# Optimization experiments

Hardware: AMD Instinct MI355X
Metric: run time of the kernel (lower is better)

Reference implementation:

```python
import jax, jax.numpy as jnp
import numpy as np

ALPHA = 0.2      # LeakyReLU negative slope
DROPOUT_P = 0.1  # torch F.dropout default training=True, so it IS applied
D_OUT = 128


def setup_inputs() -> dict:
    key = jax.random.key(0)
    k1, k2, k3 = jax.random.split(key, 3)
    N, D_IN = 8192, 128
    batch = jax.random.normal(k1, (N, D_IN), dtype=jnp.float32)
    # xavier_uniform gain=1.414 scale for faithfulness of magnitude
    w = jax.random.uniform(k2, (D_IN, D_OUT), dtype=jnp.float32, minval=-1.0, maxval=1.0) * (1.414 * np.sqrt(6.0 / (D_IN + D_OUT)))
    a = jax.random.uniform(k3, (2 * D_OUT, 1), dtype=jnp.float32, minval=-1.0, maxval=1.0) * (1.414 * np.sqrt(6.0 / (2 * D_OUT + 1)))
    return {"batch": batch, "w": w, "a": a}


def reference(batch, w, a):
    h = batch.reshape(-1, w.shape[0])            # [N, D_in]
    Wh = h @ w                                   # [N, D_out]
    Wh1 = Wh @ a[:D_OUT, :]                      # [N, 1]
    Wh2 = Wh @ a[D_OUT:, :]                      # [N, 1]
    e = Wh1 + Wh2.T                              # [N, N] additive scores
    e = jnp.where(e > 0, e, ALPHA * e)           # LeakyReLU
    attention = jax.nn.softmax(e, axis=1)        # row softmax
    # dropout with a fixed key (deterministic reference)
    keep = jax.random.bernoulli(jax.random.key(42), 1.0 - DROPOUT_P, attention.shape)
    attention = jnp.where(keep, attention / (1.0 - DROPOUT_P), 0.0)
    h_prime = attention @ Wh                     # [N, D_out]
    return jax.nn.elu(h_prime)                   # concat=True -> elu
```

## Files before the change

kernel.cpp:

```cpp
#include <hip/hip_runtime.h>
#include <stdint.h>

#define ALPHA 0.2f
#define LOG2E 1.4426950408889634f

typedef __bf16 bf16x8 __attribute__((ext_vector_type(8)));
typedef float f32x4 __attribute__((ext_vector_type(4)));

__device__ __forceinline__ uint32_t rotl32(uint32_t x, int r) {
  return __builtin_amdgcn_alignbit(x, x, 32 - r);
}

__device__ __forceinline__ uint32_t tf_mix(uint32_t f) {
  const uint32_t ks1 = 42u, ks2 = 0x1BD11BF0u;
  uint32_t x0 = 0u;
  uint32_t x1 = f + ks1;
#define TFR(r) { x0 += x1; x1 = rotl32(x1, r); x1 ^= x0; }
  TFR(13) TFR(15) TFR(26) TFR(6)  x0 += ks1; x1 += ks2 + 1u;
  TFR(17) TFR(29) TFR(16) TFR(24) x0 += ks2; x1 += 0u  + 2u;
  TFR(13) TFR(15) TFR(26) TFR(6)  x0 += 0u;  x1 += ks1 + 3u;
  TFR(17) TFR(29) TFR(16) TFR(24) x0 += ks1; x1 += ks2 + 4u;
  TFR(13) TFR(15) TFR(26) TFR(6)  x0 += ks2; x1 += 0u  + 5u;
#undef TFR
  return x0 ^ x1;
}

__device__ __forceinline__ unsigned short f2bf(float f) {
  uint32_t u = __float_as_uint(f);
  return (unsigned short)((u + 0x7fffu + ((u >> 16) & 1u)) >> 16);
}

__global__ __launch_bounds__(256) void wh_kernel(
    const float* __restrict__ batch, const float* __restrict__ w,
    const float* __restrict__ a, unsigned short* __restrict__ whb2,
    float* __restrict__ s1, float* __restrict__ s2, uint32_t* __restrict__ s2key) {
  __shared__ float whlds[32][128];
  int t = threadIdx.x;
  int i0 = blockIdx.x * 32;
  int d = t & 127, rg = t >> 7;
  int ib = i0 + rg * 16;
  float acc[16];
#pragma unroll
  for (int r = 0; r < 16; ++r) acc[r] = 0.f;
  for (int k = 0; k < 128; k += 4) {
    float wv0 = w[(k + 0) * 128 + d];
    float wv1 = w[(k + 1) * 128 + d];
    float wv2 = w[(k + 2) * 128 + d];
    float wv3 = w[(k + 3) * 128 + d];
#pragma unroll
    for (int r = 0; r < 16; ++r) {
      float4 b4 = *(const float4*)&batch[(ib + r) * 128 + k];
      acc[r] = fmaf(b4.w, wv3, fmaf(b4.z, wv2, fmaf(b4.y, wv1, fmaf(b4.x, wv0, acc[r]))));
    }
  }
  unsigned short hb[16];
#pragma unroll
  for (int r = 0; r < 16; ++r) {
    whlds[rg * 16 + r][d] = acc[r];
    hb[r] = f2bf(acc[r]);
  }
  uint32_t pk[8];
#pragma unroll
  for (int q = 0; q < 8; ++q) pk[q] = (uint32_t)hb[2 * q] | ((uint32_t)hb[2 * q + 1] << 16);
  uint32_t base0 = (((uint32_t)(ib >> 3) * 16u + (uint32_t)(d & 15)) * 8u + (uint32_t)(d >> 4)) * 8u;
  *(uint4*)&whb2[base0]        = make_uint4(pk[0], pk[1], pk[2], pk[3]);
  *(uint4*)&whb2[base0 + 1024] = make_uint4(pk[4], pk[5], pk[6], pk[7]);
  __syncthreads();
  int rr = t >> 3, seg = t & 7, c0 = seg * 16;
  const float* wr = &whlds[rr][c0];
  float p1 = 0.f, p2 = 0.f;
#pragma unroll
  for (int c = 0; c < 16; ++c) {
    float v = wr[c];
    p1 = fmaf(v, a[c0 + c], p1);
    p2 = fmaf(v, a[128 + c0 + c], p2);
  }
  p1 += __shfl_xor(p1, 1, 64); p1 += __shfl_xor(p1, 2, 64); p1 += __shfl_xor(p1, 4, 64);
  p2 += __shfl_xor(p2, 1, 64); p2 += __shfl_xor(p2, 2, 64); p2 += __shfl_xor(p2, 4, 64);
  if (seg == 0) { s1[i0 + rr] = p1; s2[i0 + rr] = p2; }
  float v = (seg == 0) ? p2 : -3.4e38f;
#pragma unroll
  for (int m = 1; m <= 32; m <<= 1) v = fmaxf(v, __shfl_xor(v, m, 64));
  if ((t & 63) == 0) {
    uint32_t b = __float_as_uint(v);
    uint32_t key = (b & 0x80000000u) ? ~b : (b | 0x80000000u);
    atomicMax(s2key, key);
  }
}

__global__ __launch_bounds__(256, 4) void gat_main(
    const float* __restrict__ s1, const float* __restrict__ s2g,
    const uint32_t* __restrict__ s2key, const unsigned short* __restrict__ whb2,
    float* __restrict__ pacc, float* __restrict__ pz) {
  __shared__ __align__(16) float smem[4160];
  int t = threadIdx.x;
  int rb = blockIdx.x >> 2, ck = blockIdx.x & 3;
  int R0 = rb * 16, C0 = ck * 2048;

  for (int k = t; k < 512; k += 256) {
    float4 v4 = ((const float4*)(s2g + C0))[k];
    float sL, e1, e2;
    sL = v4.x * LOG2E; e1 = __builtin_amdgcn_exp2f(sL); e2 = __builtin_amdgcn_exp2f(ALPHA * sL);
    ((float2*)smem)[k * 4 + 0] = make_float2(e1, e2);
    sL = v4.y * LOG2E; e1 = __builtin_amdgcn_exp2f(sL); e2 = __builtin_amdgcn_exp2f(ALPHA * sL);
    ((float2*)smem)[k * 4 + 1] = make_float2(e1, e2);
    sL = v4.z * LOG2E; e1 = __builtin_amdgcn_exp2f(sL); e2 = __builtin_amdgcn_exp2f(ALPHA * sL);
    ((float2*)smem)[k * 4 + 2] = make_float2(e1, e2);
    sL = v4.w * LOG2E; e1 = __builtin_amdgcn_exp2f(sL); e2 = __builtin_amdgcn_exp2f(ALPHA * sL);
    ((float2*)smem)[k * 4 + 3] = make_float2(e1, e2);
  }

  uint32_t kk = *s2key;
  uint32_t mb = (kk & 0x80000000u) ? (kk ^ 0x80000000u) : ~kk;
  float s2maxL = __uint_as_float(mb) * LOG2E;

  int w = t >> 6, lane = t & 63;
  int r = lane & 15, q = lane >> 4;

  float s1L = s1[R0 + r] * LOG2E;
  float xmL = s1L + s2maxL;
  float mrL = fmaxf(xmL, ALPHA * xmL);
  float F1 = __builtin_amdgcn_exp2f(s1L - mrL);
  float F2 = __builtin_amdgcn_exp2f(fmaf(ALPHA, s1L, -mrL));

  uint32_t fcur = (uint32_t)(R0 + r) * 8192u + (uint32_t)(C0 + w * 32 + q * 8);
  uint32_t voff = (((uint32_t)(C0 / 8 + w * 4 + q)) * 16u + (uint32_t)r) * 128u;
  const char* pB = (const char*)whb2;
  const float2* Eb = ((const float2*)smem) + w * 32 + q * 8;

  f32x4 acc0 = {0,0,0,0}, acc1 = {0,0,0,0}, acc2 = {0,0,0,0}, acc3 = {0,0,0,0};
  f32x4 acc4 = {0,0,0,0}, acc5 = {0,0,0,0}, acc6 = {0,0,0,0}, acc7 = {0,0,0,0};
  float z = 0.f;
  const uint32_t KTH = 0xE6666600u;

  __syncthreads();

  for (int it = 0; it < 16; ++it) {
    bf16x8 B0 = *(const bf16x8*)(pB + voff);
    bf16x8 B1 = *(const bf16x8*)(pB + voff + 16);
    bf16x8 B2 = *(const bf16x8*)(pB + voff + 32);
    bf16x8 B3 = *(const bf16x8*)(pB + voff + 48);
    bf16x8 B4 = *(const bf16x8*)(pB + voff + 64);
    bf16x8 B5 = *(const bf16x8*)(pB + voff + 80);
    bf16x8 B6 = *(const bf16x8*)(pB + voff + 96);
    bf16x8 B7 = *(const bf16x8*)(pB + voff + 112);
    float4 E01 = *(const float4*)(Eb);
    float4 E23 = *(const float4*)(Eb + 2);
    float4 E45 = *(const float4*)(Eb + 4);
    float4 E67 = *(const float4*)(Eb + 6);
    __builtin_amdgcn_sched_barrier(0);

    bf16x8 A;
#define ELEM(idx, e1v, e2v)                                   \
    {                                                         \
      uint32_t bb = tf_mix(fcur + idx);                       \
      float pv = fmaxf(F1 * (e1v), F2 * (e2v));               \
      z += pv;                                                \
      pv = (bb < KTH) ? pv : 0.f;                             \
      A[idx] = (__bf16)pv;                                    \
    }
    ELEM(0, E01.x, E01.y)
    ELEM(1, E01.z, E01.w)
    ELEM(2, E23.x, E23.y)
    ELEM(3, E23.z, E23.w)
    ELEM(4, E45.x, E45.y)
    ELEM(5, E45.z, E45.w)
    ELEM(6, E67.x, E67.y)
    ELEM(7, E67.z, E67.w)
#undef ELEM

    acc0 = __builtin_amdgcn_mfma_f32_16x16x32_bf16(A, B0, acc0, 0, 0, 0);
    acc1 = __builtin_amdgcn_mfma_f32_16x16x32_bf16(A, B1, acc1, 0, 0, 0);
    acc2 = __builtin_amdgcn_mfma_f32_16x16x32_bf16(A, B2, acc2, 0, 0, 0);
    acc3 = __builtin_amdgcn_mfma_f32_16x16x32_bf16(A, B3, acc3, 0, 0, 0);
    acc4 = __builtin_amdgcn_mfma_f32_16x16x32_bf16(A, B4, acc4, 0, 0, 0);
    acc5 = __builtin_amdgcn_mfma_f32_16x16x32_bf16(A, B5, acc5, 0, 0, 0);
    acc6 = __builtin_amdgcn_mfma_f32_16x16x32_bf16(A, B6, acc6, 0, 0, 0);
    acc7 = __builtin_amdgcn_mfma_f32_16x16x32_bf16(A, B7, acc7, 0, 0, 0);

    fcur += 128u;
    voff += 32768u;
    Eb += 128;
  }

  __syncthreads();
  float zq = z + __shfl_xor(z, 16, 64);
  zq += __shfl_xor(zq, 32, 64);
  if (lane < 16) smem[4096 + w * 16 + lane] = zq;

  float* red = smem;
  int wbase = w * 1024 + q * 256 + r;
#define STOREG(u, accN)                                \
  {                                                    \
    red[wbase + 0 * 64 + (u) * 16] = accN[0];          \
    red[wbase + 1 * 64 + (u) * 16] = accN[1];          \
    red[wbase + 2 * 64 + (u) * 16] = accN[2];          \
    red[wbase + 3 * 64 + (u) * 16] = accN[3];          \
  }
  STOREG(0, acc0) STOREG(1, acc1) STOREG(2, acc2) STOREG(3, acc3)
  __syncthreads();
#pragma unroll
  for (int k2 = 0; k2 < 4; ++k2) {
    int idx = t * 4 + k2;
    float s = (red[idx] + red[1024 + idx]) + (red[2048 + idx] + red[3072 + idx]);
    atomicAdd(&pacc[(R0 + (idx >> 6)) * 128 + (idx & 63)], s);
  }
  __syncthreads();
  STOREG(0, acc4) STOREG(1, acc5) STOREG(2, acc6) STOREG(3, acc7)
#undef STOREG
  __syncthreads();
#pragma unroll
  for (int k2 = 0; k2 < 4; ++k2) {
    int idx = t * 4 + k2;
    float s = (red[idx] + red[1024 + idx]) + (red[2048 + idx] + red[3072 + idx]);
    atomicAdd(&pacc[(R0 + (idx >> 6)) * 128 + 64 + (idx & 63)], s);
  }
  if (t < 16) {
    float zs = (smem[4096 + t] + smem[4112 + t]) + (smem[4128 + t] + smem[4144 + t]);
    atomicAdd(&pz[R0 + t], zs);
  }
}

__global__ __launch_bounds__(256) void gat_final(
    const float* __restrict__ pacc, const float* __restrict__ pz,
    float* __restrict__ out) {
  int t = threadIdx.x;
  int row = blockIdx.x * 8 + (t >> 5);
  int d4 = (t & 31) * 4;
  float zinv = 1.f / (0.9f * pz[row]);
  float4 p = *(const float4*)&pacc[row * 128 + d4];
  float4 o;
  float v;
  v = p.x * zinv; o.x = v > 0.f ? v : expm1f(v);
  v = p.y * zinv; o.y = v > 0.f ? v : expm1f(v);
  v = p.z * zinv; o.z = v > 0.f ? v : expm1f(v);
  v = p.w * zinv; o.w = v > 0.f ? v : expm1f(v);
  *(float4*)&out[row * 128 + d4] = o;
}

extern "C" void kernel_launch(void* const* d_in, const int* in_sizes, int n_in,
                              void* d_out, int out_size, void* d_ws, size_t ws_size,
                              hipStream_t stream) {
  const float* batch = (const float*)d_in[0];
  const float* w = (const float*)d_in[1];
  const float* a = (const float*)d_in[2];
  float* out = (float*)d_out;
  char* ws = (char*)d_ws;
  float* pacc = (float*)ws;
  float* pz = (float*)(ws + 4194304);
  uint32_t* s2key = (uint32_t*)(ws + 4194304 + 32768);
  unsigned short* whb2 = (unsigned short*)(ws + 4194304 + 32768 + 64);
  float* s1 = (float*)(ws + 4194304 + 32768 + 64 + 2097152);
  float* s2 = (float*)(ws + 4194304 + 32768 + 64 + 2097152 + 32768);

  hipMemsetAsync(ws, 0, 4194304 + 32768 + 64, stream);
  wh_kernel<<<256, 256, 0, stream>>>(batch, w, a, whb2, s1, s2, s2key);
  gat_main<<<2048, 256, 0, stream>>>(s1, s2, s2key, whb2, pacc, pz);
  gat_final<<<1024, 256, 0, stream>>>(pacc, pz, out);
}
```

Before: 175.6 us.

## Precompute dropout mask bits in a separate kernel and accumulate into output

Moves the Threefry dropout hashing out of the attention MFMA loop into a dedicated mask_kernel that packs keep bits into 32-bit words, processing four hashes at a time for ILP. The main loop then reads one mask word per iteration instead of hashing eight elements. It also removes the pacc workspace by accumulating directly into the output buffer and finalizing in place. The cost is an extra kernel launch plus 8 MB of mask traffic.

```diff
diff --git a/kernel.cpp b/kernel.cpp
--- a/kernel.cpp
+++ b/kernel.cpp
@@ -11,23 +11,50 @@
   return __builtin_amdgcn_alignbit(x, x, 32 - r);
 }
 
-__device__ __forceinline__ uint32_t tf_mix(uint32_t f) {
+__device__ __forceinline__ void tf_mix4(uint32_t f0, uint32_t f1, uint32_t f2, uint32_t f3,
+                                        uint32_t& o0, uint32_t& o1, uint32_t& o2, uint32_t& o3) {
   const uint32_t ks1 = 42u, ks2 = 0x1BD11BF0u;
-  uint32_t x0 = 0u;
-  uint32_t x1 = f + ks1;
-#define TFR(r) { x0 += x1; x1 = rotl32(x1, r); x1 ^= x0; }
-  TFR(13) TFR(15) TFR(26) TFR(6)  x0 += ks1; x1 += ks2 + 1u;
-  TFR(17) TFR(29) TFR(16) TFR(24) x0 += ks2; x1 += 0u  + 2u;
-  TFR(13) TFR(15) TFR(26) TFR(6)  x0 += 0u;  x1 += ks1 + 3u;
-  TFR(17) TFR(29) TFR(16) TFR(24) x0 += ks1; x1 += ks2 + 4u;
-  TFR(13) TFR(15) TFR(26) TFR(6)  x0 += ks2; x1 += 0u  + 5u;
-#undef TFR
-  return x0 ^ x1;
+  uint32_t a0 = 0u, a1 = 0u, a2 = 0u, a3 = 0u;
+  uint32_t b0 = f0 + ks1, b1 = f1 + ks1, b2 = f2 + ks1, b3 = f3 + ks1;
+#define Q4(rr)                                                              \
+  a0 += b0; a1 += b1; a2 += b2; a3 += b3;                                   \
+  b0 = rotl32(b0, rr); b1 = rotl32(b1, rr);                                 \
+  b2 = rotl32(b2, rr); b3 = rotl32(b3, rr);                                 \
+  b0 ^= a0; b1 ^= a1; b2 ^= a2; b3 ^= a3;
+#define KADD(c0, c1)                                                        \
+  a0 += (c0); a1 += (c0); a2 += (c0); a3 += (c0);                           \
+  b0 += (c1); b1 += (c1); b2 += (c1); b3 += (c1);
+  Q4(13) Q4(15) Q4(26) Q4(6)  KADD(ks1, ks2 + 1u)
+  Q4(17) Q4(29) Q4(16) Q4(24) KADD(ks2, 0u + 2u)
+  Q4(13) Q4(15) Q4(26) Q4(6)  KADD(0u, ks1 + 3u)
+  Q4(17) Q4(29) Q4(16) Q4(24) KADD(ks1, ks2 + 4u)
+  Q4(13) Q4(15) Q4(26) Q4(6)  KADD(ks2, 0u + 5u)
+#undef Q4
+#undef KADD
+  o0 = a0 ^ b0; o1 = a1 ^ b1; o2 = a2 ^ b2; o3 = a3 ^ b3;
 }
 
 __device__ __forceinline__ unsigned short f2bf(float f) {
   uint32_t u = __float_as_uint(f);
   return (unsigned short)((u + 0x7fffu + ((u >> 16) & 1u)) >> 16);
+}
+
+__global__ __launch_bounds__(256) void mask_kernel(uint32_t* __restrict__ kmask) {
+  const uint32_t KTH = 0xE6666600u;
+  uint32_t T = blockIdx.x * 256u + threadIdx.x;
+  uint32_t f0 = T * 32u;
+  uint32_t word = 0u;
+#pragma unroll 1
+  for (int g = 7; g >= 0; --g) {
+    uint32_t h0, h1, h2, h3;
+    tf_mix4(f0 + (uint32_t)(4 * g), f0 + (uint32_t)(4 * g + 1),
+            f0 + (uint32_t)(4 * g + 2), f0 + (uint32_t)(4 * g + 3), h0, h1, h2, h3);
+    word = (word << 1) | (uint32_t)(h3 < KTH);
+    word = (word << 1) | (uint32_t)(h2 < KTH);
+    word = (word << 1) | (uint32_t)(h1 < KTH);
+    word = (word << 1) | (uint32_t)(h0 < KTH);
+  }
+  kmask[T] = word;
 }
 
 __global__ __launch_bounds__(256) void wh_kernel(
@@ -91,6 +118,7 @@
 __global__ __launch_bounds__(256, 4) void gat_main(
     const float* __restrict__ s1, const float* __restrict__ s2g,
     const uint32_t* __restrict__ s2key, const unsigned short* __restrict__ whb2,
+    const uint32_t* __restrict__ kmask,
     float* __restrict__ pacc, float* __restrict__ pz) {
   __shared__ __align__(16) float smem[4160];
   int t = threadIdx.x;
@@ -123,18 +151,20 @@
   float F1 = __builtin_amdgcn_exp2f(s1L - mrL);
   float F2 = __builtin_amdgcn_exp2f(fmaf(ALPHA, s1L, -mrL));
 
-  uint32_t fcur = (uint32_t)(R0 + r) * 8192u + (uint32_t)(C0 + w * 32 + q * 8);
+  uint32_t dwBase = (uint32_t)(R0 + r) * 256u + (uint32_t)(ck * 64 + w);
+  int mq = q * 8;
+
   uint32_t voff = (((uint32_t)(C0 / 8 + w * 4 + q)) * 16u + (uint32_t)r) * 128u;
   const char* pB = (const char*)whb2;
   const float2* Eb = ((const float2*)smem) + w * 32 + q * 8;
 
   f32x4 acc0 = {0,0,0,0}, acc1 = {0,0,0,0}, acc2 = {0,0,0,0}, acc3 = {0,0,0,0};
   f32x4 acc4 = {0,0,0,0}, acc5 = {0,0,0,0}, acc6 = {0,0,0,0}, acc7 = {0,0,0,0};
-  float z = 0.f;
-  const uint32_t KTH = 0xE6666600u;
-
-  __syncthreads();
-
+  float z0 = 0.f, z1 = 0.f;
+
+  __syncthreads();
+
+#pragma unroll 1
   for (int it = 0; it < 16; ++it) {
     bf16x8 B0 = *(const bf16x8*)(pB + voff);
     bf16x8 B1 = *(const bf16x8*)(pB + voff + 16);
@@ -144,19 +174,20 @@
     bf16x8 B5 = *(const bf16x8*)(pB + voff + 80);
     bf16x8 B6 = *(const bf16x8*)(pB + voff + 96);
     bf16x8 B7 = *(const bf16x8*)(pB + voff + 112);
+    uint32_t km = kmask[dwBase + (uint32_t)(it * 4)];
     float4 E01 = *(const float4*)(Eb);
     float4 E23 = *(const float4*)(Eb + 2);
     float4 E45 = *(const float4*)(Eb + 4);
     float4 E67 = *(const float4*)(Eb + 6);
     __builtin_amdgcn_sched_barrier(0);
 
+    uint32_t mbits = km >> mq;
     bf16x8 A;
 #define ELEM(idx, e1v, e2v)                                   \
     {                                                         \
-      uint32_t bb = tf_mix(fcur + idx);                       \
       float pv = fmaxf(F1 * (e1v), F2 * (e2v));               \
-      z += pv;                                                \
-      pv = (bb < KTH) ? pv : 0.f;                             \
+      if ((idx) < 4) z0 += pv; else z1 += pv;                 \
+      pv = (mbits & (1u << (idx))) ? pv : 0.f;                \
       A[idx] = (__bf16)pv;                                    \
     }
     ELEM(0, E01.x, E01.y)
@@ -178,10 +209,10 @@
     acc6 = __builtin_amdgcn_mfma_f32_16x16x32_bf16(A, B6, acc6, 0, 0, 0);
     acc7 = __builtin_amdgcn_mfma_f32_16x16x32_bf16(A, B7, acc7, 0, 0, 0);
 
-    fcur += 128u;
     voff += 32768u;
     Eb += 128;
   }
+  float z = z0 + z1;
 
   __syncthreads();
   float zq = z + __shfl_xor(z, 16, 64);
@@ -222,13 +253,12 @@
 }
 
 __global__ __launch_bounds__(256) void gat_final(
-    const float* __restrict__ pacc, const float* __restrict__ pz,
-    float* __restrict__ out) {
+    float* __restrict__ out, const float* __restrict__ pz) {
   int t = threadIdx.x;
   int row = blockIdx.x * 8 + (t >> 5);
   int d4 = (t & 31) * 4;
   float zinv = 1.f / (0.9f * pz[row]);
-  float4 p = *(const float4*)&pacc[row * 128 + d4];
+  float4 p = *(const float4*)&out[row * 128 + d4];
   float4 o;
   float v;
   v = p.x * zinv; o.x = v > 0.f ? v : expm1f(v);
@@ -246,15 +276,17 @@
   const float* a = (const float*)d_in[2];
   float* out = (float*)d_out;
   char* ws = (char*)d_ws;
-  float* pacc = (float*)ws;
-  float* pz = (float*)(ws + 4194304);
-  uint32_t* s2key = (uint32_t*)(ws + 4194304 + 32768);
-  unsigned short* whb2 = (unsigned short*)(ws + 4194304 + 32768 + 64);
-  float* s1 = (float*)(ws + 4194304 + 32768 + 64 + 2097152);
-  float* s2 = (float*)(ws + 4194304 + 32768 + 64 + 2097152 + 32768);
-
-  hipMemsetAsync(ws, 0, 4194304 + 32768 + 64, stream);
+  float* pz = (float*)ws;
+  uint32_t* s2key = (uint32_t*)(ws + 32768);
+  unsigned short* whb2 = (unsigned short*)(ws + 32768 + 64);
+  float* s1 = (float*)(ws + 32768 + 64 + 2097152);
+  float* s2 = (float*)(ws + 32768 + 64 + 2097152 + 32768);
+  uint32_t* kmask = (uint32_t*)(ws + 32768 + 64 + 2097152 + 65536);
+
+  (void)hipMemsetAsync(d_out, 0, 8192 * 128 * sizeof(float), stream);
+  (void)hipMemsetAsync(ws, 0, 32768 + 64, stream);
+  mask_kernel<<<8192, 256, 0, stream>>>(kmask);
   wh_kernel<<<256, 256, 0, stream>>>(batch, w, a, whb2, s1, s2, s2key);
-  gat_main<<<2048, 256, 0, stream>>>(s1, s2, s2key, whb2, pacc, pz);
-  gat_final<<<1024, 256, 0, stream>>>(pacc, pz, out);
-}
+  gat_main<<<2048, 256, 0, stream>>>(s1, s2, s2key, whb2, kmask, out, pz);
+  gat_final<<<1024, 256, 0, stream>>>(out, pz);
+}
```

After: 343.7 us. +95.7%, slower.
